# Kernel tuning notes

Measured on AMD Instinct MI355X. Metric: run time of the kernel, lower is better.

Reference implementation:

```python
import math
import jax, jax.numpy as jnp
import numpy as np

B, T, D = 4, 2048, 1024
H, DH = 16, 64
FF = 4096
EPS = 1e-5


def setup_inputs() -> dict:
    key = jax.random.key(0)
    ks = jax.random.split(key, 12)
    s = 0.02
    inp = {
        "x": jax.random.normal(ks[0], (B, T, D), dtype=jnp.float32),
        "ln1_g": jnp.ones((D,), jnp.float32),
        "ln1_b": jnp.zeros((D,), jnp.float32),
        "ln2_g": jnp.ones((D,), jnp.float32),
        "ln2_b": jnp.zeros((D,), jnp.float32),
        # torch nn.Linear convention: weight shape [out, in], y = x @ W.T + b
        "wq": jax.random.normal(ks[1], (D, D), jnp.float32) * s,
        "bq": jnp.zeros((D,), jnp.float32),
        "wk": jax.random.normal(ks[2], (D, D), jnp.float32) * s,
        "bk": jnp.zeros((D,), jnp.float32),
        "wv": jax.random.normal(ks[3], (D, D), jnp.float32) * s,
        "bv": jnp.zeros((D,), jnp.float32),
        "wo": jax.random.normal(ks[4], (D, D), jnp.float32) * s,
        "bo": jnp.zeros((D,), jnp.float32),
        "w1": jax.random.normal(ks[5], (FF, D), jnp.float32) * s,
        "b1": jnp.zeros((FF,), jnp.float32),
        "w2": jax.random.normal(ks[6], (D, FF), jnp.float32) * s,
        "b2": jnp.zeros((D,), jnp.float32),
    }
    return inp


def _layernorm(h, g, b):
    mu = jnp.mean(h, axis=-1, keepdims=True)
    var = jnp.mean(jnp.square(h - mu), axis=-1, keepdims=True)
    return (h - mu) * jax.lax.rsqrt(var + EPS) * g + b


def _block(x, ln1_g, ln1_b, ln2_g, ln2_b, wq, bq, wk, bk, wv, bv, wo, bo, w1, b1, w2, b2):
    b, t, d = x.shape
    h = _layernorm(x, ln1_g, ln1_b)
    q = (h @ wq.T + bq).reshape(b, t, H, DH)
    k = (h @ wk.T + bk).reshape(b, t, H, DH)
    v = (h @ wv.T + bv).reshape(b, t, H, DH)
    # full (non-causal) attention, as in the torch module
    att = jnp.einsum("bqhd,bkhd->bhqk", q, k) / math.sqrt(DH)
    att = jax.nn.softmax(att, axis=-1)
    out = jnp.einsum("bhqk,bkhd->bqhd", att, v).reshape(b, t, d)
    x = x + (out @ wo.T + bo)
    h2 = _layernorm(x, ln2_g, ln2_b)
    ff = jax.nn.gelu(h2 @ w1.T + b1, approximate=False) @ w2.T + b2
    return x + ff


def reference(x, ln1_g, ln1_b, ln2_g, ln2_b, wq, bq, wk, bk, wv, bv, wo, bo, w1, b1, w2, b2):
    return _block(x, ln1_g, ln1_b, ln2_g, ln2_b, wq, bq, wk, bk, wv, bv, wo, bo, w1, b1, w2, b2)
```

## Files before the change

### kernel.cpp

```cpp
#include <hip/hip_runtime.h>
#include <cstdint>
#include <cstddef>

typedef __attribute__((ext_vector_type(8))) __bf16 bf16x8;
typedef __attribute__((ext_vector_type(4))) float f32x4;
typedef __attribute__((ext_vector_type(8))) unsigned short us8;
typedef __attribute__((ext_vector_type(4))) unsigned short us4;

__device__ inline unsigned short f2bf(float f) {
    unsigned int u = __float_as_uint(f);
    u += 0x7fffu + ((u >> 16) & 1u);
    return (unsigned short)(u >> 16);
}

__device__ inline unsigned int pkbf_t(float hi, float lo) {
    return __builtin_amdgcn_perm(__float_as_uint(hi), __float_as_uint(lo), 0x07060302u);
}

__device__ inline void async_copy16(const void* g, void* l) {
    __builtin_amdgcn_global_load_lds(
        (const __attribute__((address_space(1))) unsigned int*)g,
        (__attribute__((address_space(3))) unsigned int*)l, 16, 0, 0);
}

__global__ __launch_bounds__(256) void cvt_bf16(const float* __restrict__ in,
                                                unsigned short* __restrict__ out, int n4) {
    int i = blockIdx.x * 256 + threadIdx.x;
    if (i < n4) {
        float4 v = ((const float4*)in)[i];
        us4 o;
        o[0] = f2bf(v.x); o[1] = f2bf(v.y); o[2] = f2bf(v.z); o[3] = f2bf(v.w);
        ((us4*)out)[i] = o;
    }
}

__global__ __launch_bounds__(256) void ln_bf16(const float* __restrict__ X,
                                               const float* __restrict__ g,
                                               const float* __restrict__ b,
                                               unsigned short* __restrict__ out) {
    int row = blockIdx.x;
    int t = threadIdx.x;
    float4 v = ((const float4*)(X + (size_t)row * 1024))[t];
    float s  = v.x + v.y + v.z + v.w;
    float s2 = v.x * v.x + v.y * v.y + v.z * v.z + v.w * v.w;
#pragma unroll
    for (int m = 1; m < 64; m <<= 1) {
        s  += __shfl_xor(s, m, 64);
        s2 += __shfl_xor(s2, m, 64);
    }
    __shared__ float red[8];
    int w = t >> 6, l = t & 63;
    if (l == 0) { red[w] = s; red[4 + w] = s2; }
    __syncthreads();
    s  = red[0] + red[1] + red[2] + red[3];
    s2 = red[4] + red[5] + red[6] + red[7];
    float mu  = s * (1.0f / 1024.0f);
    float var = s2 * (1.0f / 1024.0f) - mu * mu;
    float rs  = rsqrtf(var + 1e-5f);
    int c = t * 4;
    float4 gv = *(const float4*)(g + c);
    float4 bv = *(const float4*)(b + c);
    us4 o;
    o[0] = f2bf((v.x - mu) * rs * gv.x + bv.x);
    o[1] = f2bf((v.y - mu) * rs * gv.y + bv.y);
    o[2] = f2bf((v.z - mu) * rs * gv.z + bv.z);
    o[3] = f2bf((v.w - mu) * rs * gv.w + bv.w);
    *(us4*)(out + (size_t)row * 1024 + c) = o;
}

#define BM 128
#define BN 128
#define BK 32

template <int EPI>
__global__ __launch_bounds__(256) void gemm_nt(const unsigned short* __restrict__ A,
                                               const unsigned short* __restrict__ B,
                                               const float* __restrict__ bias,
                                               const float* __restrict__ resid,
                                               void* __restrict__ Cout, int N, int K) {
    __shared__ __align__(16) unsigned short As[BM * BK];
    __shared__ __align__(16) unsigned short Bs[BN * BK];
    const int tid = threadIdx.x;
    const int lane = tid & 63, w = tid >> 6;
    const int quad = lane >> 4, l16 = lane & 15;
    const int wr = w >> 1, wc = w & 1;
    const size_t bm = (size_t)blockIdx.y * BM;
    const size_t bn = (size_t)blockIdx.x * BN;

    f32x4 acc[4][4];
#pragma unroll
    for (int i = 0; i < 4; i++)
#pragma unroll
        for (int j = 0; j < 4; j++) acc[i][j] = (f32x4){0.f, 0.f, 0.f, 0.f};

    for (int k0 = 0; k0 < K; k0 += BK) {
#pragma unroll
        for (int i = 0; i < 2; i++) {
            int e = (i * 256 + tid) * 8;
            int r = e >> 5, c = e & 31;
            async_copy16(A + (bm + r) * K + k0 + c, &As[e]);
            async_copy16(B + (bn + r) * K + k0 + c, &Bs[e]);
        }
        __syncthreads();
        bf16x8 af[4], bfr[4];
#pragma unroll
        for (int mt = 0; mt < 4; mt++)
            af[mt] = *(const bf16x8*)&As[(wr * 64 + mt * 16 + l16) * BK + quad * 8];
#pragma unroll
        for (int nt = 0; nt < 4; nt++)
            bfr[nt] = *(const bf16x8*)&Bs[(wc * 64 + nt * 16 + l16) * BK + quad * 8];
#pragma unroll
        for (int mt = 0; mt < 4; mt++)
#pragma unroll
            for (int nt = 0; nt < 4; nt++)
                acc[mt][nt] = __builtin_amdgcn_mfma_f32_16x16x32_bf16(af[mt], bfr[nt],
                                                                      acc[mt][nt], 0, 0, 0);
        __syncthreads();
    }

#pragma unroll
    for (int mt = 0; mt < 4; mt++) {
#pragma unroll
        for (int nt = 0; nt < 4; nt++) {
#pragma unroll
            for (int r = 0; r < 4; r++) {
                size_t row = bm + wr * 64 + mt * 16 + quad * 4 + r;
                size_t col = bn + wc * 64 + nt * 16 + l16;
                float v = acc[mt][nt][r] + bias[col];
                if (EPI == 1) {
                    v = 0.5f * v * (1.0f + erff(v * 0.70710678118654752f));
                    ((unsigned short*)Cout)[row * N + col] = f2bf(v);
                } else if (EPI == 2) {
                    ((float*)Cout)[row * N + col] = v + resid[row * N + col];
                } else if (EPI == 6) {
                    int sel = (int)(bn >> 10);
                    if (sel == 0) {
                        ((unsigned short*)Cout)[row * 1024 + col] =
                            f2bf(v * 0.18033688011112042f);
                    } else {
                        int key = (int)row & 2047;
                        int bh  = (((int)row >> 11) << 4) | (((int)col >> 6) & 15);
                        int dh  = (int)col & 63;
                        size_t addr;
                        if (sel == 1)
                            addr = 8388608 + (size_t)bh * 131072 +
                                   (size_t)(key >> 6) * 4096 + (size_t)(key & 63) * 64 +
                                   ((((dh >> 3) ^ (key & 7))) << 3) + (dh & 7);
                        else
                            addr = 16777216 + (size_t)bh * 131072 +
                                   (size_t)(key >> 6) * 4096 + (size_t)dh * 64 +
                                   (((((key >> 3) & 7) ^ (dh & 7))) << 3) + (key & 7);
                        ((unsigned short*)Cout)[addr] = f2bf(v);
                    }
                }
            }
        }
    }
}

__global__ __launch_bounds__(256) void attn_kernel(const unsigned short* __restrict__ Q,
                                                   const unsigned short* __restrict__ Kb,
                                                   const unsigned short* __restrict__ Vtb,
                                                   unsigned short* __restrict__ O) {
    const int bh   = blockIdx.x >> 4;
    const int qblk = blockIdx.x & 15;
    const int b = bh >> 4, h = bh & 15;
    const int tid = threadIdx.x, lane = tid & 63, w = tid >> 6;
    const int quad = lane >> 4, l16 = lane & 15;
    const int sw = l16 & 7;

    __shared__ __align__(16) unsigned short smem[20480];
    unsigned short* Vts = smem + 8192;
    unsigned short* Psw = smem + 12288 + w * 2048;

    const size_t qrow0 = (size_t)b * 2048 + (size_t)qblk * 128 + w * 32;
    const int hcol = h * 64;

    bf16x8 qfr[2][2];
#pragma unroll
    for (int qf = 0; qf < 2; qf++)
#pragma unroll
        for (int kp = 0; kp < 2; kp++)
            qfr[qf][kp] = *(const bf16x8*)(Q + (qrow0 + qf * 16 + l16) * 1024 +
                                           hcol + kp * 32 + quad * 8);

    const unsigned short* ksrc = Kb  + (size_t)bh * 131072;
    const unsigned short* vsrc = Vtb + (size_t)bh * 131072;

    async_copy16(ksrc + tid * 8,        smem + tid * 8);
    async_copy16(ksrc + 2048 + tid * 8, smem + 2048 + tid * 8);
    async_copy16(vsrc + tid * 8,        Vts + tid * 8);
    async_copy16(vsrc + 2048 + tid * 8, Vts + 2048 + tid * 8);

    f32x4 acc[4][2];
#pragma unroll
    for (int df = 0; df < 4; df++)
#pragma unroll
        for (int qf = 0; qf < 2; qf++) acc[df][qf] = (f32x4){0.f, 0.f, 0.f, 0.f};
    float l_[2] = {0.f, 0.f};

    for (int kt = 0; kt < 32; ++kt) {
        unsigned short* Ks = (kt & 1) ? (smem + 4096) : smem;
        if (kt < 31) {
            unsigned short* Kd = (kt & 1) ? smem : (smem + 4096);
            const unsigned short* kg = ksrc + (size_t)(kt + 1) * 4096;
            async_copy16(kg + tid * 8,        Kd + tid * 8);
            async_copy16(kg + 2048 + tid * 8, Kd + 2048 + tid * 8);
            asm volatile("s_waitcnt vmcnt(4)" ::: "memory");
        } else {
            asm volatile("s_waitcnt vmcnt(2)" ::: "memory");
        }
        asm volatile("s_barrier" ::: "memory");

        f32x4 s[4][2];
#pragma unroll
        for (int mf = 0; mf < 4; mf++)
#pragma unroll
            for (int qf = 0; qf < 2; qf++) s[mf][qf] = (f32x4){0.f, 0.f, 0.f, 0.f};
        __builtin_amdgcn_s_setprio(1);
#pragma unroll
        for (int kp = 0; kp < 2; kp++) {
#pragma unroll
            for (int mf = 0; mf < 4; mf++) {
                bf16x8 kf = *(const bf16x8*)&Ks[(mf * 16 + l16) * 64 +
                                                (((kp * 4 + quad) ^ sw) << 3)];
#pragma unroll
                for (int qf = 0; qf < 2; qf++)
                    s[mf][qf] = __builtin_amdgcn_mfma_f32_16x16x32_bf16(kf, qfr[qf][kp],
                                                                        s[mf][qf], 0, 0, 0);
            }
        }
        __builtin_amdgcn_s_setprio(0);

#pragma unroll
        for (int mf = 0; mf < 4; mf++)
#pragma unroll
            for (int qf = 0; qf < 2; qf++) {
                float e0 = exp2f(s[mf][qf][0]);
                float e1 = exp2f(s[mf][qf][1]);
                float e2 = exp2f(s[mf][qf][2]);
                float e3 = exp2f(s[mf][qf][3]);
                l_[qf] += (e0 + e1) + (e2 + e3);
                *(uint2*)&Psw[(qf * 16 + l16) * 64 +
                              (((mf * 2 + (quad >> 1)) ^ sw) << 3) + ((quad & 1) << 2)] =
                    make_uint2(pkbf_t(e1, e0), pkbf_t(e3, e2));
            }
        asm volatile("s_waitcnt lgkmcnt(0)" ::: "memory");

        if (kt < 31) {
            asm volatile("s_waitcnt vmcnt(2)" ::: "memory");
        } else {
            asm volatile("s_waitcnt vmcnt(0)" ::: "memory");
        }
        asm volatile("s_barrier" ::: "memory");

        __builtin_amdgcn_s_setprio(1);
#pragma unroll
        for (int kp = 0; kp < 2; kp++) {
            bf16x8 pf[2];
#pragma unroll
            for (int qf = 0; qf < 2; qf++)
                pf[qf] = *(const bf16x8*)&Psw[(qf * 16 + l16) * 64 +
                                              (((kp * 4 + quad) ^ sw) << 3)];
#pragma unroll
            for (int df = 0; df < 4; df++) {
                bf16x8 vf = *(const bf16x8*)&Vts[(df * 16 + l16) * 64 +
                                                 (((kp * 4 + quad) ^ sw) << 3)];
#pragma unroll
                for (int qf = 0; qf < 2; qf++)
                    acc[df][qf] = __builtin_amdgcn_mfma_f32_16x16x32_bf16(vf, pf[qf],
                                                                          acc[df][qf], 0, 0, 0);
            }
        }
        __builtin_amdgcn_s_setprio(0);

        asm volatile("s_barrier" ::: "memory");
        if (kt < 31) {
            const unsigned short* vg = vsrc + (size_t)(kt + 1) * 4096;
            async_copy16(vg + tid * 8,        Vts + tid * 8);
            async_copy16(vg + 2048 + tid * 8, Vts + 2048 + tid * 8);
        }
    }

#pragma unroll
    for (int qf = 0; qf < 2; qf++) {
        l_[qf] += __shfl_xor(l_[qf], 16, 64);
        l_[qf] += __shfl_xor(l_[qf], 32, 64);
    }

    __syncthreads();
    float inv[2] = {1.f / l_[0], 1.f / l_[1]};
    unsigned short* Ls = smem;
#pragma unroll
    for (int df = 0; df < 4; df++)
#pragma unroll
        for (int qf = 0; qf < 2; qf++)
#pragma unroll
            for (int r = 0; r < 4; r++) {
                int dh = df * 16 + quad * 4 + r;
                int q  = w * 32 + qf * 16 + l16;
                Ls[dh * 130 + q] =
                    (unsigned short)((__float_as_uint(acc[df][qf][r] * inv[qf]) + 0x8000u) >> 16);
            }
    __syncthreads();
    int q = tid >> 1, dh0 = (tid & 1) * 32;
    size_t obase = ((size_t)b * 2048 + (size_t)qblk * 128 + q) * 1024 + hcol + dh0;
#pragma unroll
    for (int c = 0; c < 4; c++) {
        us8 o;
#pragma unroll
        for (int j = 0; j < 8; j++) o[j] = Ls[(dh0 + c * 8 + j) * 130 + q];
        *(us8*)(O + obase + c * 8) = o;
    }
}

extern "C" void kernel_launch(void* const* d_in, const int* in_sizes, int n_in,
                              void* d_out, int out_size, void* d_ws, size_t ws_size,
                              hipStream_t stream) {
    const float* x     = (const float*)d_in[0];
    const float* ln1_g = (const float*)d_in[1];
    const float* ln1_b = (const float*)d_in[2];
    const float* ln2_g = (const float*)d_in[3];
    const float* ln2_b = (const float*)d_in[4];
    const float* wq = (const float*)d_in[5];
    const float* bq = (const float*)d_in[6];
    const float* wk = (const float*)d_in[7];
    const float* bk = (const float*)d_in[8];
    const float* wv = (const float*)d_in[9];
    const float* bv = (const float*)d_in[10];
    const float* wo = (const float*)d_in[11];
    const float* bo = (const float*)d_in[12];
    const float* w1 = (const float*)d_in[13];
    const float* b1 = (const float*)d_in[14];
    const float* w2 = (const float*)d_in[15];
    const float* b2 = (const float*)d_in[16];

    const size_t MB = 1u << 20;
    char* ws = (char*)d_ws;
    unsigned short* wqkvb = (unsigned short*)(ws + 0 * MB);
    unsigned short* wob  = (unsigned short*)(ws + 6 * MB);
    unsigned short* w1b  = (unsigned short*)(ws + 8 * MB);
    unsigned short* w2b  = (unsigned short*)(ws + 16 * MB);
    unsigned short* hb   = (unsigned short*)(ws + 24 * MB);
    unsigned short* qkvb = (unsigned short*)(ws + 40 * MB);
    unsigned short* qb   = qkvb;
    unsigned short* kblk = qkvb + 8388608;
    unsigned short* vtblk= qkvb + 16777216;
    float*          x1   = (float*)(ws + 56 * MB);
    unsigned short* h2b  = (unsigned short*)(ws + 40 * MB);
    unsigned short* ff1b = (unsigned short*)(ws + 88 * MB);
    float*          bqkv = (float*)(ws + 151 * MB);

    const int D = 1024, FF = 4096, Mrows = 8192;

    cvt_bf16<<<(D * D / 4 + 255) / 256, 256, 0, stream>>>(wq, wqkvb,               D * D / 4);
    cvt_bf16<<<(D * D / 4 + 255) / 256, 256, 0, stream>>>(wk, wqkvb + D * D,       D * D / 4);
    cvt_bf16<<<(D * D / 4 + 255) / 256, 256, 0, stream>>>(wv, wqkvb + 2 * D * D,   D * D / 4);
    cvt_bf16<<<(D * D / 4 + 255) / 256, 256, 0, stream>>>(wo, wob, D * D / 4);
    cvt_bf16<<<(FF * D / 4 + 255) / 256, 256, 0, stream>>>(w1, w1b, FF * D / 4);
    cvt_bf16<<<(FF * D / 4 + 255) / 256, 256, 0, stream>>>(w2, w2b, FF * D / 4);

    hipMemcpyAsync(bqkv,            bq, D * sizeof(float), hipMemcpyDeviceToDevice, stream);
    hipMemcpyAsync(bqkv + D,        bk, D * sizeof(float), hipMemcpyDeviceToDevice, stream);
    hipMemcpyAsync(bqkv + 2 * D,    bv, D * sizeof(float), hipMemcpyDeviceToDevice, stream);

    ln_bf16<<<Mrows, 256, 0, stream>>>(x, ln1_g, ln1_b, hb);

    dim3 gQKV(3 * D / BN, Mrows / BM);
    gemm_nt<6><<<gQKV, 256, 0, stream>>>(hb, wqkvb, bqkv, nullptr, qkvb, D, D);

    attn_kernel<<<1024, 256, 0, stream>>>(qb, kblk, vtblk, hb);

    dim3 gD(D / BN, Mrows / BM);
    gemm_nt<2><<<gD, 256, 0, stream>>>(hb, wob, bo, x, x1, D, D);

    ln_bf16<<<Mrows, 256, 0, stream>>>(x1, ln2_g, ln2_b, h2b);

    dim3 gFF(FF / BN, Mrows / BM);
    gemm_nt<1><<<gFF, 256, 0, stream>>>(h2b, w1b, b1, nullptr, ff1b, FF, D);

    gemm_nt<2><<<gD, 256, 0, stream>>>(ff1b, w2b, b2, x1, (float*)d_out, D, FF);
}
```

Before: 634.3 us.

## Triple-buffer GEMM LDS tiles with async prefetch and XCD-aware block remap

Converts the bf16 GEMM main loop from single-buffered load/sync/compute into a three-stage LDS ring. The next K tile is prefetched with global_load_lds while the current one is computed, and explicit vmcnt waits plus a single barrier replace the two __syncthreads per iteration. It also remaps workgroup IDs so consecutive tiles spread across the 8 XCDs, and raises wave priority around the MFMA block. The cost is 3x the LDS per block, which may reduce occupancy. Dropping the trailing barrier relies on the three-buffer distance to avoid overwriting a tile that a slower wave is still reading.

```diff
diff --git a/kernel.cpp b/kernel.cpp
--- a/kernel.cpp
+++ b/kernel.cpp
@@ -78,14 +78,19 @@
                                                const float* __restrict__ bias,
                                                const float* __restrict__ resid,
                                                void* __restrict__ Cout, int N, int K) {
-    __shared__ __align__(16) unsigned short As[BM * BK];
-    __shared__ __align__(16) unsigned short Bs[BN * BK];
+    __shared__ __align__(16) unsigned short As[3][BM * BK];
+    __shared__ __align__(16) unsigned short Bs[3][BN * BK];
     const int tid = threadIdx.x;
     const int lane = tid & 63, w = tid >> 6;
     const int quad = lane >> 4, l16 = lane & 15;
     const int wr = w >> 1, wc = w & 1;
-    const size_t bm = (size_t)blockIdx.y * BM;
-    const size_t bn = (size_t)blockIdx.x * BN;
+
+    const int gx = gridDim.x;
+    const int nwg = gx * gridDim.y;
+    int wg = blockIdx.y * gx + blockIdx.x;
+    if (!(nwg & 7)) wg = (wg & 7) * (nwg >> 3) + (wg >> 3);
+    const size_t bm = (size_t)(wg / gx) * BM;
+    const size_t bn = (size_t)(wg % gx) * BN;
 
     f32x4 acc[4][4];
 #pragma unroll
@@ -93,29 +98,50 @@
 #pragma unroll
         for (int j = 0; j < 4; j++) acc[i][j] = (f32x4){0.f, 0.f, 0.f, 0.f};
 
-    for (int k0 = 0; k0 < K; k0 += BK) {
-#pragma unroll
-        for (int i = 0; i < 2; i++) {
-            int e = (i * 256 + tid) * 8;
-            int r = e >> 5, c = e & 31;
-            async_copy16(A + (bm + r) * K + k0 + c, &As[e]);
-            async_copy16(B + (bn + r) * K + k0 + c, &Bs[e]);
-        }
-        __syncthreads();
+    const int nk = K / BK;
+
+#pragma unroll
+    for (int i = 0; i < 2; i++) {
+        int e = (i * 256 + tid) * 8, r = e >> 5, c = e & 31;
+        async_copy16(A + (bm + r) * K + c, &As[0][e]);
+        async_copy16(B + (bn + r) * K + c, &Bs[0][e]);
+    }
+
+    int cur = 0;
+    for (int kt = 0; kt < nk; ++kt) {
+        int nxt = (cur == 2) ? 0 : cur + 1;
+        if (kt + 1 < nk) {
+            const int k0 = (kt + 1) * BK;
+#pragma unroll
+            for (int i = 0; i < 2; i++) {
+                int e = (i * 256 + tid) * 8, r = e >> 5, c = e & 31;
+                async_copy16(A + (bm + r) * K + k0 + c, &As[nxt][e]);
+                async_copy16(B + (bn + r) * K + k0 + c, &Bs[nxt][e]);
+            }
+            asm volatile("s_waitcnt vmcnt(4)" ::: "memory");
+        } else {
+            asm volatile("s_waitcnt vmcnt(0)" ::: "memory");
+        }
+        asm volatile("s_barrier" ::: "memory");
+
         bf16x8 af[4], bfr[4];
 #pragma unroll
         for (int mt = 0; mt < 4; mt++)
-            af[mt] = *(const bf16x8*)&As[(wr * 64 + mt * 16 + l16) * BK + quad * 8];
+            af[mt] = *(const bf16x8*)&As[cur][(wr * 64 + mt * 16 + l16) * BK + quad * 8];
 #pragma unroll
         for (int nt = 0; nt < 4; nt++)
-            bfr[nt] = *(const bf16x8*)&Bs[(wc * 64 + nt * 16 + l16) * BK + quad * 8];
+            bfr[nt] = *(const bf16x8*)&Bs[cur][(wc * 64 + nt * 16 + l16) * BK + quad * 8];
+
+        __builtin_amdgcn_s_setprio(1);
 #pragma unroll
         for (int mt = 0; mt < 4; mt++)
 #pragma unroll
             for (int nt = 0; nt < 4; nt++)
                 acc[mt][nt] = __builtin_amdgcn_mfma_f32_16x16x32_bf16(af[mt], bfr[nt],
                                                                       acc[mt][nt], 0, 0, 0);
-        __syncthreads();
+        __builtin_amdgcn_s_setprio(0);
+        __builtin_amdgcn_sched_barrier(0);
+        cur = nxt;
     }
 
 #pragma unroll
```

Result: faster. 603.8 us (-4.8%).
